# Optimization experiments

Hardware: AMD Instinct MI355X
Metric: run time of the kernel (lower is better)

## Reference

```python
import jax, jax.numpy as jnp
import numpy as np
import math

B, S, D, H = 4, 2048, 1024, 16
DK = D // H  # 64


def setup_inputs() -> dict:
    key = jax.random.key(0)
    ks = jax.random.split(key, 10)
    scale = 1.0 / math.sqrt(D)
    inp = {
        "context_sequence": jax.random.normal(ks[0], (B, S, D), dtype=jnp.float32),
        "value_sequence": jax.random.normal(ks[1], (B, S, D), dtype=jnp.float32),
        "mask": jax.random.randint(ks[2], (S, S), 0, 2, dtype=jnp.int32),
        # stacked per-head projection params: [H, D, DK] weights, [H, DK] biases
        "Wq": jax.random.uniform(ks[3], (H, D, DK), jnp.float32, -scale, scale),
        "bq": jnp.zeros((H, DK), jnp.float32),
        "Wk": jax.random.uniform(ks[4], (H, D, DK), jnp.float32, -scale, scale),
        "bk": jnp.zeros((H, DK), jnp.float32),
        "Wv": jax.random.uniform(ks[5], (H, D, DK), jnp.float32, -scale, scale),
        "bv": jnp.zeros((H, DK), jnp.float32),
        "Wo": jax.random.uniform(ks[6], (D, D), jnp.float32, -scale, scale),
        "bo": jnp.zeros((D,), jnp.float32),
    }
    return inp


def reference(context_sequence, value_sequence, mask, Wq, bq, Wk, bk, Wv, bv, Wo, bo):
    # per-head projections batched over heads: [B,H,S,DK]
    Q = jnp.einsum("bsd,hdk->bhsk", context_sequence, Wq) + bq[None, :, None, :]
    K = jnp.einsum("bsd,hdk->bhsk", context_sequence, Wk) + bk[None, :, None, :]
    V = jnp.einsum("bsd,hdk->bhsk", value_sequence, Wv) + bv[None, :, None, :]
    scores = jnp.einsum("bhsk,bhtk->bhst", Q, K) / math.sqrt(DK)
    scores = jnp.where(mask[None, None, :, :] == 1, jnp.float32(-1e9), scores)
    attn = jax.nn.softmax(scores, axis=-1)
    out = jnp.einsum("bhst,bhtk->bhsk", attn, V)  # [B,H,S,DK]
    concat = out.transpose(0, 2, 1, 3).reshape(B, S, D)  # heads concatenated
    # output projection (dropout is identity in eval mode)
    return concat @ Wo.T + bo
```

## Files before the change

kernel.cpp:

```cpp
#include <hip/hip_runtime.h>
#include <hip/hip_bf16.h>

#define DEVI __device__ __forceinline__

typedef __attribute__((ext_vector_type(8))) short bf16x8;
typedef __attribute__((ext_vector_type(4))) float f32x4;
typedef unsigned short u16;
typedef unsigned long long u64;


DEVI void async16(const void* g, const void* l) {
  __builtin_amdgcn_global_load_lds(
      (const __attribute__((address_space(1))) unsigned int*)g,
      (__attribute__((address_space(3))) unsigned int*)l, 16, 0, 0);
}

DEVI u16 f2bf(float x) {
  unsigned int u = __float_as_uint(x);
  return (u16)((u + 0x7fffu + ((u >> 16) & 1u)) >> 16);
}

DEVI float fast_exp2(float x) {
#if __has_builtin(__builtin_amdgcn_exp2f)
  return __builtin_amdgcn_exp2f(x);
#else
  return exp2f(x);
#endif
}

DEVI unsigned pk_bf16(unsigned hi, unsigned lo) {
#if __has_builtin(__builtin_amdgcn_perm)
  return __builtin_amdgcn_perm(hi, lo, 0x07060302u);
#else
  return (hi & 0xffff0000u) | (lo >> 16);
#endif
}

DEVI unsigned mk2(unsigned b, int k) {
  return ((((b >> k) & 1u) ? 0u : 0x0000FFFFu) | (((b >> (k + 1)) & 1u) ? 0u : 0xFFFF0000u));
}


__global__ __launch_bounds__(256) void prep_kernel(
    const float* __restrict__ ctx, const float* __restrict__ val, const int* __restrict__ msk,
    const float* __restrict__ Wq, const float* __restrict__ Wk, const float* __restrict__ Wv,
    const float* __restrict__ Wo, const float* __restrict__ bq, const float* __restrict__ bk,
    u16* __restrict__ Xc, u16* __restrict__ Xv, u16* __restrict__ Wqt, u16* __restrict__ Wkt,
    u16* __restrict__ Wvt, u16* __restrict__ WoB, u64* __restrict__ mbits, float* __restrict__ bqk) {
  __shared__ float tile[64 * 69];
  const int blk = blockIdx.x, tid = threadIdx.x;
  if (blk < 16384) {
    const float* src = (blk < 8192) ? ctx : val;
    u16* dst = (blk < 8192) ? Xc : Xv;
    int i = (blk & 8191) * 256 + tid;
    float4 v = ((const float4*)src)[i];
    ushort4 o;
    o.x = f2bf(v.x); o.y = f2bf(v.y); o.z = f2bf(v.z); o.w = f2bf(v.w);
    ((ushort4*)dst)[i] = o;
  } else if (blk < 17408) {
    int i = (blk - 16384) * 256 + tid;
    float4 v = ((const float4*)Wo)[i];
    ushort4 o;
    o.x = f2bf(v.x); o.y = f2bf(v.y); o.z = f2bf(v.z); o.w = f2bf(v.w);
    ((ushort4*)WoB)[i] = o;
  } else if (blk < 18176) {
    int t = blk - 17408;
    int mat = t >> 8, r = t & 255, h = r >> 4, d0 = (r & 15) * 64;
    const float* Ws = (mat == 0) ? Wq : (mat == 1) ? Wk : Wv;
    u16* Wd = (mat == 0) ? Wqt : (mat == 1) ? Wkt : Wvt;
    const int dg = tid & 15, rg = tid >> 4;
#pragma unroll
    for (int i = 0; i < 4; i++) {
      int dr = rg + i * 16;
      float4 v = *(const float4*)&Ws[((size_t)(h * 1024 + d0 + dr)) * 64 + dg * 4];
      tile[dr * 69 + dg * 4 + 0] = v.x;
      tile[dr * 69 + dg * 4 + 1] = v.y;
      tile[dr * 69 + dg * 4 + 2] = v.z;
      tile[dr * 69 + dg * 4 + 3] = v.w;
    }
    __syncthreads();
#pragma unroll
    for (int i = 0; i < 4; i++) {
      int k = rg + i * 16;
      ushort4 o;
      o.x = f2bf(tile[(dg * 4 + 0) * 69 + k]);
      o.y = f2bf(tile[(dg * 4 + 1) * 69 + k]);
      o.z = f2bf(tile[(dg * 4 + 2) * 69 + k]);
      o.w = f2bf(tile[(dg * 4 + 3) * 69 + k]);
      *(ushort4*)&Wd[(size_t)(h * 64 + k) * 1024 + d0 + dg * 4] = o;
    }
  } else if (blk < 34560) {
    int gid = (blk - 18176) * 256 + tid;
    u64 bal = __ballot(msk[gid] == 1);
    if ((tid & 63) == 0) mbits[(size_t)((gid >> 6) & 31) * 2048 + (gid >> 11)] = bal;
  } else {
    int i = (blk - 34560) * 256 + tid;
    bqk[i] = (i < 1024) ? bq[i] : bk[i - 1024];
  }
}


__global__ __launch_bounds__(256) void qkv_gemm(const u16* __restrict__ Xc, const u16* __restrict__ Xv,
                                                const u16* __restrict__ Wqkt, const u16* __restrict__ Wvt,
                                                const float* __restrict__ bqk, const float* __restrict__ bvv,
                                                u16* __restrict__ QKb, u16* __restrict__ Vtg, float qscale) {
  __shared__ __align__(16) u16 As[2][128 * 32];
  __shared__ __align__(16) u16 Bs[2][128 * 32];
  const int tid = threadIdx.x;
  const int w = tid >> 6, lane = tid & 63, quad = lane >> 4, lc = lane & 15;
  const int K = 1024;
  const bool isV = blockIdx.y >= 16;
  const int m0 = blockIdx.x * 128;
  const int n0 = (isV ? (blockIdx.y - 16) : blockIdx.y) * 128;
  const u16* A  = isV ? Xv : Xc;
  const u16* Bt = isV ? Wvt : Wqkt;
  const float* bias = isV ? bvv : bqk;
  const int wrow = (w >> 1) * 64, wcol = (w & 1) * 64;
  const int srow = tid >> 2, sc = tid & 3;
  const u16* Ag = A + (size_t)(m0 + srow) * K + sc * 8;
  const u16* Bg = Bt + (size_t)(n0 + srow) * K + sc * 8;

  async16(Ag, As[0] + w * 512);
  async16(Ag + (size_t)64 * K, As[0] + w * 512 + 2048);
  async16(Bg, Bs[0] + w * 512);
  async16(Bg + (size_t)64 * K, Bs[0] + w * 512 + 2048);

  f32x4 acc[4][4] = {};
  for (int k0 = 0; k0 < K; k0 += 32) {
    const int cur = (k0 >> 5) & 1;
    __syncthreads();
    if (k0 + 32 < K) {
      async16(Ag + k0 + 32, As[cur ^ 1] + w * 512);
      async16(Ag + k0 + 32 + (size_t)64 * K, As[cur ^ 1] + w * 512 + 2048);
      async16(Bg + k0 + 32, Bs[cur ^ 1] + w * 512);
      async16(Bg + k0 + 32 + (size_t)64 * K, Bs[cur ^ 1] + w * 512 + 2048);
    }
    bf16x8 af[4], bfr[4];
#pragma unroll
    for (int rt = 0; rt < 4; rt++) af[rt] = *(const bf16x8*)&As[cur][(wrow + rt * 16 + lc) * 32 + quad * 8];
#pragma unroll
    for (int ct = 0; ct < 4; ct++) bfr[ct] = *(const bf16x8*)&Bs[cur][(wcol + ct * 16 + lc) * 32 + quad * 8];
#pragma unroll
    for (int rt = 0; rt < 4; rt++)
#pragma unroll
      for (int ct = 0; ct < 4; ct++)
        acc[rt][ct] = __builtin_amdgcn_mfma_f32_16x16x32_bf16(af[rt], bfr[ct], acc[rt][ct], 0, 0, 0);
  }
#pragma unroll
  for (int ct = 0; ct < 4; ct++) {
    int col = n0 + wcol + ct * 16 + lc;
    float bv = bias[col];
    float os = (!isV && col < 1024) ? qscale : 1.0f;
#pragma unroll
    for (int rt = 0; rt < 4; rt++) {
      if (isV) {
        int trow = m0 + wrow + rt * 16 + quad * 4;
        ushort4 pk;
        pk.x = f2bf(acc[rt][ct][0] + bv);
        pk.y = f2bf(acc[rt][ct][1] + bv);
        pk.z = f2bf(acc[rt][ct][2] + bv);
        pk.w = f2bf(acc[rt][ct][3] + bv);
        size_t off = ((size_t)(trow >> 11) * 1024 + col) * 2048 + (trow & 2047);
        *(ushort4*)(Vtg + off) = pk;
      } else {
#pragma unroll
        for (int r = 0; r < 4; r++) {
          int row = m0 + wrow + rt * 16 + quad * 4 + r;
          QKb[(size_t)row * 2048 + col] = f2bf((acc[rt][ct][r] + bv) * os);
        }
      }
    }
  }
}


__global__ __launch_bounds__(256, 2) void attn_kernel(const u16* __restrict__ QK, const u16* __restrict__ Vt,
                                                      const u64* __restrict__ mbits, u16* __restrict__ AO) {
  __shared__ __align__(16) u16 SM[16384];
  __shared__ uint4 Tbl[256];
  const int S = 2048, D = 1024, QS = 2048;
  const int tid = threadIdx.x, w = tid >> 6, lane = tid & 63, quad = lane >> 4, lc = lane & 15;
  const int q0 = blockIdx.x * 256;
  const int b = blockIdx.y >> 4, h = blockIdx.y & 15;
  const size_t baseq = (size_t)b * S * QS + (size_t)h * 64;
  const size_t vbase = (size_t)blockIdx.y * 64 * S;
  const int sr = lane >> 3, gch = (lane & 7) ^ sr, lx = lc & 7;

  {
    unsigned bv = (unsigned)tid;
    uint4 e;
    e.x = mk2(bv, 0); e.y = mk2(bv, 2); e.z = mk2(bv, 4); e.w = mk2(bv, 6);
    Tbl[bv] = e;
  }

#pragma unroll
  for (int i = 0; i < 8; i++) {
    const u16* g = QK + baseq + (size_t)(q0 + w * 64 + i * 8 + sr) * QS + gch * 8;
    async16(g, SM + w * 4096 + i * 512);
  }
  const int kperm = 32 * (w & 1) + 4 * (w >> 1) + 8 * (sr >> 2) + (sr & 3);
  const u16* Kg0 = QK + baseq + 1024 + (size_t)kperm * QS + gch * 8;
  const u16* Vg0 = Vt + vbase + (size_t)(w * 16 + sr) * S + gch * 8;
  __syncthreads();

  bf16x8 aq[4][2];
#pragma unroll
  for (int s = 0; s < 4; s++)
#pragma unroll
    for (int ks = 0; ks < 2; ks++)
      aq[s][ks] = *(const bf16x8*)&SM[w * 4096 + (s * 16 + lc) * 64 + (((ks * 4 + quad) ^ lx) << 3)];
  __syncthreads();

  async16(Kg0, SM + w * 1024);
  async16(Kg0 + (size_t)16 * QS, SM + w * 1024 + 512);
  async16(Vg0, SM + 8192 + w * 1024);
  async16(Vg0 + (size_t)8 * S, SM + 8192 + w * 1024 + 512);

  const u64* mptr = mbits + (size_t)(q0 + w * 64 + lc);
  const int sh8 = quad << 3;

  bf16x8 ones;
#pragma unroll
  for (int j = 0; j < 8; j++) ones[j] = (short)0x3F80;

  const f32x4 z = {};
  f32x4 acco[4][4] = {};
  f32x4 accl[4] = {};

  for (int t0 = 0; t0 < S; t0 += 64) {
    const int cur = (t0 >> 6) & 1;
    const u16* Kc = SM + cur * 4096;
    const u16* Vc = SM + 8192 + cur * 4096;
    __syncthreads();
    if (t0 + 64 < S) {
      u16* Kn = SM + (cur ^ 1) * 4096;
      u16* Vn = SM + 8192 + (cur ^ 1) * 4096;
      const u16* Kg = Kg0 + (size_t)(t0 + 64) * QS;
      const u16* Vg = Vg0 + (t0 + 64);
      async16(Kg, Kn + w * 1024);
      async16(Kg + (size_t)16 * QS, Kn + w * 1024 + 512);
      async16(Vg, Vn + w * 1024);
      async16(Vg + (size_t)8 * S, Vn + w * 1024 + 512);
    }

    u64 mw0 = mptr[(size_t)(t0 >> 6) * 2048];
    u64 mw1 = mptr[(size_t)(t0 >> 6) * 2048 + 16];
    u64 mw2 = mptr[(size_t)(t0 >> 6) * 2048 + 32];
    u64 mw3 = mptr[(size_t)(t0 >> 6) * 2048 + 48];

    bf16x8 bk0[4], bk1[4];
#pragma unroll
    for (int ct = 0; ct < 4; ct++) {
      bk0[ct] = *(const bf16x8*)&Kc[(ct * 16 + lc) * 64 + ((quad ^ lx) << 3)];
      bk1[ct] = *(const bf16x8*)&Kc[(ct * 16 + lc) * 64 + (((4 + quad) ^ lx) << 3)];
    }
    f32x4 sacc[4][4];
    __builtin_amdgcn_s_setprio(1);
#pragma unroll
    for (int s = 0; s < 4; s++)
#pragma unroll
      for (int ct = 0; ct < 4; ct++)
        sacc[s][ct] = __builtin_amdgcn_mfma_f32_16x16x32_bf16(bk0[ct], aq[s][0], z, 0, 0, 0);
#pragma unroll
    for (int s = 0; s < 4; s++)
#pragma unroll
      for (int ct = 0; ct < 4; ct++)
        sacc[s][ct] = __builtin_amdgcn_mfma_f32_16x16x32_bf16(bk1[ct], aq[s][1], sacc[s][ct], 0, 0, 0);
    __builtin_amdgcn_s_setprio(0);

    bf16x8 bv0[4], bv1[4];
#pragma unroll
    for (int ct = 0; ct < 4; ct++) {
      bv0[ct] = *(const bf16x8*)&Vc[(ct * 16 + lc) * 64 + ((quad ^ lx) << 3)];
      bv1[ct] = *(const bf16x8*)&Vc[(ct * 16 + lc) * 64 + (((4 + quad) ^ lx) << 3)];
    }

#pragma unroll
    for (int s = 0; s < 4; s++) {
      const u64 mw = (s == 0) ? mw0 : (s == 1) ? mw1 : (s == 2) ? mw2 : mw3;
      uint4 ma = Tbl[((unsigned)mw >> sh8) & 255u];
      uint4 mb = Tbl[((unsigned)(mw >> 32) >> sh8) & 255u];
      unsigned pu[4][4];
#pragma unroll
      for (int ct = 0; ct < 4; ct++)
#pragma unroll
        for (int r = 0; r < 4; r++)
          pu[ct][r] = __float_as_uint(fast_exp2(sacc[s][ct][r]));
      union { unsigned u[4]; bf16x8 v; } f0, f1;
      f0.u[0] = pk_bf16(pu[0][1], pu[0][0]) & ma.x;
      f0.u[1] = pk_bf16(pu[0][3], pu[0][2]) & ma.y;
      f0.u[2] = pk_bf16(pu[2][1], pu[2][0]) & ma.z;
      f0.u[3] = pk_bf16(pu[2][3], pu[2][2]) & ma.w;
      f1.u[0] = pk_bf16(pu[1][1], pu[1][0]) & mb.x;
      f1.u[1] = pk_bf16(pu[1][3], pu[1][2]) & mb.y;
      f1.u[2] = pk_bf16(pu[3][1], pu[3][0]) & mb.z;
      f1.u[3] = pk_bf16(pu[3][3], pu[3][2]) & mb.w;

      __builtin_amdgcn_s_setprio(1);
#pragma unroll
      for (int ct = 0; ct < 4; ct++)
        acco[s][ct] = __builtin_amdgcn_mfma_f32_16x16x32_bf16(f0.v, bv0[ct], acco[s][ct], 0, 0, 0);
      accl[s] = __builtin_amdgcn_mfma_f32_16x16x32_bf16(f0.v, ones, accl[s], 0, 0, 0);
#pragma unroll
      for (int ct = 0; ct < 4; ct++)
        acco[s][ct] = __builtin_amdgcn_mfma_f32_16x16x32_bf16(f1.v, bv1[ct], acco[s][ct], 0, 0, 0);
      accl[s] = __builtin_amdgcn_mfma_f32_16x16x32_bf16(f1.v, ones, accl[s], 0, 0, 0);
      __builtin_amdgcn_s_setprio(0);
    }
  }

#pragma unroll
  for (int s = 0; s < 4; s++)
#pragma unroll
    for (int r = 0; r < 4; r++) {
      float inv = 1.0f / accl[s][r];
      size_t row = (size_t)b * S + q0 + w * 64 + s * 16 + quad * 4 + r;
#pragma unroll
      for (int ct = 0; ct < 4; ct++)
        AO[row * D + h * 64 + ct * 16 + lc] = f2bf(acco[s][ct][r] * inv);
    }
}


__global__ __launch_bounds__(256) void out_gemm(const u16* __restrict__ A, const u16* __restrict__ Bt,
                                                const float* __restrict__ bias, float* __restrict__ C) {
  __shared__ __align__(16) u16 As[2][128 * 32];
  __shared__ __align__(16) u16 Bs[2][128 * 32];
  const int tid = threadIdx.x;
  const int w = tid >> 6, lane = tid & 63, quad = lane >> 4, lc = lane & 15;
  const int K = 1024, N = 1024;
  const int m0 = blockIdx.x * 128, n0 = blockIdx.y * 128;
  const int wrow = (w >> 1) * 64, wcol = (w & 1) * 64;
  const int srow = tid >> 2, sc = tid & 3;
  const u16* Ag = A + (size_t)(m0 + srow) * K + sc * 8;
  const u16* Bg = Bt + (size_t)(n0 + srow) * K + sc * 8;

  async16(Ag, As[0] + w * 512);
  async16(Ag + (size_t)64 * K, As[0] + w * 512 + 2048);
  async16(Bg, Bs[0] + w * 512);
  async16(Bg + (size_t)64 * K, Bs[0] + w * 512 + 2048);

  f32x4 acc[4][4] = {};
  for (int k0 = 0; k0 < K; k0 += 32) {
    const int cur = (k0 >> 5) & 1;
    __syncthreads();
    if (k0 + 32 < K) {
      async16(Ag + k0 + 32, As[cur ^ 1] + w * 512);
      async16(Ag + k0 + 32 + (size_t)64 * K, As[cur ^ 1] + w * 512 + 2048);
      async16(Bg + k0 + 32, Bs[cur ^ 1] + w * 512);
      async16(Bg + k0 + 32 + (size_t)64 * K, Bs[cur ^ 1] + w * 512 + 2048);
    }
    bf16x8 af[4], bfr[4];
#pragma unroll
    for (int rt = 0; rt < 4; rt++) af[rt] = *(const bf16x8*)&As[cur][(wrow + rt * 16 + lc) * 32 + quad * 8];
#pragma unroll
    for (int ct = 0; ct < 4; ct++) bfr[ct] = *(const bf16x8*)&Bs[cur][(wcol + ct * 16 + lc) * 32 + quad * 8];
#pragma unroll
    for (int rt = 0; rt < 4; rt++)
#pragma unroll
      for (int ct = 0; ct < 4; ct++)
        acc[rt][ct] = __builtin_amdgcn_mfma_f32_16x16x32_bf16(af[rt], bfr[ct], acc[rt][ct], 0, 0, 0);
  }
#pragma unroll
  for (int ct = 0; ct < 4; ct++) {
    int col = n0 + wcol + ct * 16 + lc;
    float bv = bias[col];
#pragma unroll
    for (int rt = 0; rt < 4; rt++)
#pragma unroll
      for (int r = 0; r < 4; r++) {
        int row = m0 + wrow + rt * 16 + quad * 4 + r;
        C[(size_t)row * N + col] = acc[rt][ct][r] + bv;
      }
  }
}


extern "C" void kernel_launch(void* const* d_in, const int* in_sizes, int n_in,
                              void* d_out, int out_size, void* d_ws, size_t ws_size,
                              hipStream_t stream) {
  const int B = 4, S = 2048, D = 1024;
  const float* ctx = (const float*)d_in[0];
  const float* val = (const float*)d_in[1];
  const int*   msk = (const int*)d_in[2];
  const float* Wq  = (const float*)d_in[3];
  const float* bq  = (const float*)d_in[4];
  const float* Wk  = (const float*)d_in[5];
  const float* bk  = (const float*)d_in[6];
  const float* Wv  = (const float*)d_in[7];
  const float* bv  = (const float*)d_in[8];
  const float* Wo  = (const float*)d_in[9];
  const float* bo  = (const float*)d_in[10];
  float* out = (float*)d_out;

  char* ws = (char*)d_ws;
  size_t off = 0;
  auto alloc = [&](size_t sz) { void* p = ws + off; off += (sz + 255) & ~255ULL; return p; };
  const size_t NTOK = (size_t)B * S * D;
  u16* Xc  = (u16*)alloc(NTOK * 2);
  u16* Xv  = (u16*)alloc(NTOK * 2);
  u16* Wqt = (u16*)alloc((size_t)D * D * 2);
  u16* Wkt = (u16*)alloc((size_t)D * D * 2);
  u16* Wvt = (u16*)alloc((size_t)D * D * 2);
  u16* WoB = (u16*)alloc((size_t)D * D * 2);
  u16* QKb = (u16*)alloc(NTOK * 4);
  u16* Vtg = (u16*)alloc(NTOK * 2);
  u64* mbits = (u64*)alloc((size_t)S * S / 8);
  float* bqk = (float*)alloc(2048 * 4);
  u16* AO = Xc;
  if (off > ws_size) return;

  const float qscale = 0.125f * 1.44269504088896f;

  prep_kernel<<<34568, 256, 0, stream>>>(ctx, val, msk, Wq, Wk, Wv, Wo, bq, bk,
                                         Xc, Xv, Wqt, Wkt, Wvt, WoB, mbits, bqk);

  qkv_gemm<<<dim3(B * S / 128, 24), 256, 0, stream>>>(Xc, Xv, Wqt, Wvt, bqk, bv, QKb, Vtg, qscale);

  attn_kernel<<<dim3(S / 256, B * 16), 256, 0, stream>>>(QKb, Vtg, mbits, AO);

  out_gemm<<<dim3(B * S / 128, D / 128), 256, 0, stream>>>(AO, WoB, bo, out);
}
```

Before: 318.7 us.

## Use three-stage LDS pipeline with explicit vmcnt waits in projection GEMMs

Both the QKV projection GEMM and the output GEMM move from a double-buffered LDS scheme to a triple-buffered one, keeping two k-tiles of async global-to-LDS loads in flight. Each iteration waits with an explicit s_waitcnt vmcnt(4) rather than a full drain, then uses a raw s_barrier and a scheduling barrier. This hides more global load latency behind MFMA work. In exchange it uses more LDS per block, which may lower occupancy, and it depends on the hand-counted vmcnt being correct.

```diff
diff --git a/kernel.cpp b/kernel.cpp
--- a/kernel.cpp
+++ b/kernel.cpp
@@ -104,8 +104,8 @@
                                                 const u16* __restrict__ Wqkt, const u16* __restrict__ Wvt,
                                                 const float* __restrict__ bqk, const float* __restrict__ bvv,
                                                 u16* __restrict__ QKb, u16* __restrict__ Vtg, float qscale) {
-  __shared__ __align__(16) u16 As[2][128 * 32];
-  __shared__ __align__(16) u16 Bs[2][128 * 32];
+  __shared__ __align__(16) u16 As[3][4096];
+  __shared__ __align__(16) u16 Bs[3][4096];
   const int tid = threadIdx.x;
   const int w = tid >> 6, lane = tid & 63, quad = lane >> 4, lc = lane & 15;
   const int K = 1024;
@@ -120,32 +120,46 @@
   const u16* Ag = A + (size_t)(m0 + srow) * K + sc * 8;
   const u16* Bg = Bt + (size_t)(n0 + srow) * K + sc * 8;
 
-  async16(Ag, As[0] + w * 512);
-  async16(Ag + (size_t)64 * K, As[0] + w * 512 + 2048);
-  async16(Bg, Bs[0] + w * 512);
-  async16(Bg + (size_t)64 * K, Bs[0] + w * 512 + 2048);
+#define QKV_STAGE(buf, k)                                    \
+  do {                                                       \
+    async16(Ag + (k), As[buf] + w * 512);                    \
+    async16(Ag + (k) + (size_t)64 * K, As[buf] + w * 512 + 2048); \
+    async16(Bg + (k), Bs[buf] + w * 512);                    \
+    async16(Bg + (k) + (size_t)64 * K, Bs[buf] + w * 512 + 2048); \
+  } while (0)
+
+  QKV_STAGE(0, 0);
+  QKV_STAGE(1, 32);
 
   f32x4 acc[4][4] = {};
+  int cur = 0;
   for (int k0 = 0; k0 < K; k0 += 32) {
-    const int cur = (k0 >> 5) & 1;
-    __syncthreads();
     if (k0 + 32 < K) {
-      async16(Ag + k0 + 32, As[cur ^ 1] + w * 512);
-      async16(Ag + k0 + 32 + (size_t)64 * K, As[cur ^ 1] + w * 512 + 2048);
-      async16(Bg + k0 + 32, Bs[cur ^ 1] + w * 512);
-      async16(Bg + k0 + 32 + (size_t)64 * K, Bs[cur ^ 1] + w * 512 + 2048);
-    }
+      asm volatile("s_waitcnt vmcnt(4)" ::: "memory");
+    } else {
+      asm volatile("s_waitcnt vmcnt(0)" ::: "memory");
+    }
+    __builtin_amdgcn_s_barrier();
+    __builtin_amdgcn_sched_barrier(0);
+    if (k0 + 64 < K) {
+      int nb = cur + 2; if (nb >= 3) nb -= 3;
+      QKV_STAGE(nb, k0 + 64);
+    }
+    const u16* Ac = As[cur];
+    const u16* Bc = Bs[cur];
     bf16x8 af[4], bfr[4];
 #pragma unroll
-    for (int rt = 0; rt < 4; rt++) af[rt] = *(const bf16x8*)&As[cur][(wrow + rt * 16 + lc) * 32 + quad * 8];
-#pragma unroll
-    for (int ct = 0; ct < 4; ct++) bfr[ct] = *(const bf16x8*)&Bs[cur][(wcol + ct * 16 + lc) * 32 + quad * 8];
+    for (int rt = 0; rt < 4; rt++) af[rt] = *(const bf16x8*)&Ac[(wrow + rt * 16 + lc) * 32 + quad * 8];
+#pragma unroll
+    for (int ct = 0; ct < 4; ct++) bfr[ct] = *(const bf16x8*)&Bc[(wcol + ct * 16 + lc) * 32 + quad * 8];
 #pragma unroll
     for (int rt = 0; rt < 4; rt++)
 #pragma unroll
       for (int ct = 0; ct < 4; ct++)
         acc[rt][ct] = __builtin_amdgcn_mfma_f32_16x16x32_bf16(af[rt], bfr[ct], acc[rt][ct], 0, 0, 0);
-  }
+    cur = (cur == 2) ? 0 : cur + 1;
+  }
+#undef QKV_STAGE
 #pragma unroll
   for (int ct = 0; ct < 4; ct++) {
     int col = n0 + wcol + ct * 16 + lc;
@@ -324,8 +338,8 @@
 
 __global__ __launch_bounds__(256) void out_gemm(const u16* __restrict__ A, const u16* __restrict__ Bt,
                                                 const float* __restrict__ bias, float* __restrict__ C) {
-  __shared__ __align__(16) u16 As[2][128 * 32];
-  __shared__ __align__(16) u16 Bs[2][128 * 32];
+  __shared__ __align__(16) u16 As[3][4096];
+  __shared__ __align__(16) u16 Bs[3][4096];
   const int tid = threadIdx.x;
   const int w = tid >> 6, lane = tid & 63, quad = lane >> 4, lc = lane & 15;
   const int K = 1024, N = 1024;
@@ -335,32 +349,46 @@
   const u16* Ag = A + (size_t)(m0 + srow) * K + sc * 8;
   const u16* Bg = Bt + (size_t)(n0 + srow) * K + sc * 8;
 
-  async16(Ag, As[0] + w * 512);
-  async16(Ag + (size_t)64 * K, As[0] + w * 512 + 2048);
-  async16(Bg, Bs[0] + w * 512);
-  async16(Bg + (size_t)64 * K, Bs[0] + w * 512 + 2048);
+#define OUT_STAGE(buf, k)                                    \
+  do {                                                       \
+    async16(Ag + (k), As[buf] + w * 512);                    \
+    async16(Ag + (k) + (size_t)64 * K, As[buf] + w * 512 + 2048); \
+    async16(Bg + (k), Bs[buf] + w * 512);                    \
+    async16(Bg + (k) + (size_t)64 * K, Bs[buf] + w * 512 + 2048); \
+  } while (0)
+
+  OUT_STAGE(0, 0);
+  OUT_STAGE(1, 32);
 
   f32x4 acc[4][4] = {};
+  int cur = 0;
   for (int k0 = 0; k0 < K; k0 += 32) {
-    const int cur = (k0 >> 5) & 1;
-    __syncthreads();
     if (k0 + 32 < K) {
-      async16(Ag + k0 + 32, As[cur ^ 1] + w * 512);
-      async16(Ag + k0 + 32 + (size_t)64 * K, As[cur ^ 1] + w * 512 + 2048);
-      async16(Bg + k0 + 32, Bs[cur ^ 1] + w * 512);
-      async16(Bg + k0 + 32 + (size_t)64 * K, Bs[cur ^ 1] + w * 512 + 2048);
-    }
+      asm volatile("s_waitcnt vmcnt(4)" ::: "memory");
+    } else {
+      asm volatile("s_waitcnt vmcnt(0)" ::: "memory");
+    }
+    __builtin_amdgcn_s_barrier();
+    __builtin_amdgcn_sched_barrier(0);
+    if (k0 + 64 < K) {
+      int nb = cur + 2; if (nb >= 3) nb -= 3;
+      OUT_STAGE(nb, k0 + 64);
+    }
+    const u16* Ac = As[cur];
+    const u16* Bc = Bs[cur];
     bf16x8 af[4], bfr[4];
 #pragma unroll
-    for (int rt = 0; rt < 4; rt++) af[rt] = *(const bf16x8*)&As[cur][(wrow + rt * 16 + lc) * 32 + quad * 8];
-#pragma unroll
-    for (int ct = 0; ct < 4; ct++) bfr[ct] = *(const bf16x8*)&Bs[cur][(wcol + ct * 16 + lc) * 32 + quad * 8];
+    for (int rt = 0; rt < 4; rt++) af[rt] = *(const bf16x8*)&Ac[(wrow + rt * 16 + lc) * 32 + quad * 8];
+#pragma unroll
+    for (int ct = 0; ct < 4; ct++) bfr[ct] = *(const bf16x8*)&Bc[(wcol + ct * 16 + lc) * 32 + quad * 8];
 #pragma unroll
     for (int rt = 0; rt < 4; rt++)
 #pragma unroll
       for (int ct = 0; ct < 4; ct++)
         acc[rt][ct] = __builtin_amdgcn_mfma_f32_16x16x32_bf16(af[rt], bfr[ct], acc[rt][ct], 0, 0, 0);
-  }
+    cur = (cur == 2) ? 0 : cur + 1;
+  }
+#undef OUT_STAGE
 #pragma unroll
   for (int ct = 0; ct < 4; ct++) {
     int col = n0 + wcol + ct * 16 + lc;
```

Measured after the change: 328.8 us. 3.2% more time.
